# Kernel optimization log

Hardware: AMD Instinct MI355X
Metric: run time of the kernel (lower is better)

The kernel has to match this reference:

```python
import jax, jax.numpy as jnp
import numpy as np

B, T, HID = 2, 2048, 1536
H, HKV, D = 12, 2, 128
EPS = 1e-6
NEG = -1e9


def setup_inputs() -> dict:
    key = jax.random.key(0)
    ks = jax.random.split(key, 8)
    # rotary embeddings built from real angles (cos/sin of position*inv_freq)
    inv_freq = 1.0 / (10000.0 ** (jnp.arange(0, D, 2, dtype=jnp.float32) / D))  # [D/2]
    pos = jnp.arange(T, dtype=jnp.float32)
    ang = pos[:, None] * inv_freq[None, :]                       # [T, D/2]
    emb = jnp.concatenate([ang, ang], axis=-1)                   # [T, D]
    cos = jnp.broadcast_to(jnp.cos(emb)[None], (B, T, D))
    sin = jnp.broadcast_to(jnp.sin(emb)[None], (B, T, D))
    # additive causal mask [1,1,T,T]
    causal = jnp.tril(jnp.ones((T, T), dtype=bool))
    attention_mask = jnp.where(causal, 0.0, NEG).astype(jnp.float32)[None, None]
    s = 0.02
    return {
        "hidden_states": jax.random.normal(ks[0], (B, T, HID), jnp.float32),
        "cos": cos,
        "sin": sin,
        "attention_mask": attention_mask,
        "q_w": jax.random.normal(ks[1], (H * D, HID), jnp.float32) * s,
        "k_w": jax.random.normal(ks[2], (HKV * D, HID), jnp.float32) * s,
        "v_w": jax.random.normal(ks[3], (HKV * D, HID), jnp.float32) * s,
        "o_w": jax.random.normal(ks[4], (HID, H * D), jnp.float32) * s,
        "q_norm_w": jnp.ones((D,), jnp.float32),
        "k_norm_w": jnp.ones((D,), jnp.float32),
    }


def _rms_norm(x, w):
    # per-head RMSNorm over last dim (head_dim), computed in fp32
    xf = x.astype(jnp.float32)
    var = jnp.mean(xf * xf, axis=-1, keepdims=True)
    return (w * (xf * jax.lax.rsqrt(var + EPS))).astype(x.dtype)


def _rotate_half(x):
    x1, x2 = jnp.split(x, 2, axis=-1)
    return jnp.concatenate([-x2, x1], axis=-1)


def reference(hidden_states, cos, sin, attention_mask, q_w, k_w, v_w, o_w, q_norm_w, k_norm_w):
    b, t, _ = hidden_states.shape
    n_rep = H // HKV
    scale = D ** -0.5

    # projections -> [B, n_heads, T, D]
    q = (hidden_states @ q_w.T).reshape(b, t, H, D)
    k = (hidden_states @ k_w.T).reshape(b, t, HKV, D)
    v = (hidden_states @ v_w.T).reshape(b, t, HKV, D).transpose(0, 2, 1, 3)

    # per-head QK RMSNorm, then to [B, H, T, D]
    q = _rms_norm(q, q_norm_w).transpose(0, 2, 1, 3)
    k = _rms_norm(k, k_norm_w).transpose(0, 2, 1, 3)

    # RoPE (cos/sin broadcast over head axis)
    c = cos[:, None, :, :]
    s = sin[:, None, :, :]
    q = q * c + _rotate_half(q) * s
    k = k * c + _rotate_half(k) * s

    # GQA repeat_kv: [B, HKV, T, D] -> [B, H, T, D]
    k = jnp.repeat(k, n_rep, axis=1)
    v = jnp.repeat(v, n_rep, axis=1)

    attn = jnp.einsum('bhqd,bhkd->bhqk', q, k) * scale + attention_mask
    attn = jax.nn.softmax(attn.astype(jnp.float32), axis=-1).astype(q.dtype)
    out = jnp.einsum('bhqk,bhkd->bhqd', attn, v)
    out = out.transpose(0, 2, 1, 3).reshape(b, t, H * D)
    return out @ o_w.T
```

## Files before the change

### kernel.cpp

```cpp
#include <hip/hip_runtime.h>
#include <hip/hip_bf16.h>


#define B_   2
#define T_   2048
#define HID_ 1536
#define H_   12
#define HKV_ 2
#define D_   128
#define GQ_  (H_ / HKV_)
#define NQKV_ 2048
#define SCALE_ 0.08838834764831845f

typedef unsigned short u16;
typedef __attribute__((ext_vector_type(4))) float f32x4;
typedef __attribute__((ext_vector_type(8))) short bf16x8;
typedef __attribute__((ext_vector_type(4))) unsigned short u16x4;
typedef __attribute__((ext_vector_type(8))) unsigned short u16x8;

__device__ __forceinline__ u16 f2b(float f) {
  union { __hip_bfloat16 h; u16 u; } cv;
  cv.h = __float2bfloat16(f);
  return cv.u;
}
__device__ __forceinline__ float b2f(u16 u) {
  union { float f; unsigned i; } cv;
  cv.i = ((unsigned)u) << 16;
  return cv.f;
}

__device__ __forceinline__ void glds16(const u16* g, u16* l) {
  __builtin_amdgcn_global_load_lds((const __attribute__((address_space(1))) void*)g,
                                   (__attribute__((address_space(3))) void*)l, 16, 0, 0);
}

__global__ __launch_bounds__(256) void cvt_f32_bf16(const float* __restrict__ src,
                                                    u16* __restrict__ dst, int n4) {
  int i = blockIdx.x * 256 + threadIdx.x;
  const int stride = gridDim.x * 256;
  for (; i < n4; i += stride) {
    const float4 v = reinterpret_cast<const float4*>(src)[i];
    u16x4 o = {f2b(v.x), f2b(v.y), f2b(v.z), f2b(v.w)};
    reinterpret_cast<u16x4*>(dst)[i] = o;
  }
}

#define NH4_ 1572864
#define NQ4_ 589824
#define NK4_ 98304
__global__ __launch_bounds__(256) void cvt_inputs(const float* __restrict__ hidden,
                                                  const float* __restrict__ q_w,
                                                  const float* __restrict__ k_w,
                                                  const float* __restrict__ v_w,
                                                  u16* __restrict__ hidden_b,
                                                  u16* __restrict__ qkvw) {
  int i = blockIdx.x * 256 + threadIdx.x;
  const int stride = gridDim.x * 256;
  const int total = NH4_ + NQ4_ + 2 * NK4_;
  for (; i < total; i += stride) {
    float4 v;
    u16x4* dst;
    if (i < NH4_) {
      v = reinterpret_cast<const float4*>(hidden)[i];
      dst = reinterpret_cast<u16x4*>(hidden_b) + i;
    } else {
      const int j = i - NH4_;
      if (j < NQ4_) v = reinterpret_cast<const float4*>(q_w)[j];
      else if (j < NQ4_ + NK4_) v = reinterpret_cast<const float4*>(k_w)[j - NQ4_];
      else v = reinterpret_cast<const float4*>(v_w)[j - NQ4_ - NK4_];
      dst = reinterpret_cast<u16x4*>(qkvw) + j;
    }
    u16x4 o = {f2b(v.x), f2b(v.y), f2b(v.z), f2b(v.w)};
    *dst = o;
  }
}

__global__ __launch_bounds__(256) void gemm_bt(const u16* __restrict__ A,
                                               const u16* __restrict__ W,
                                               float* __restrict__ C,
                                               int M, int N, int K) {
  __shared__ __align__(16) u16 As[2][128 * 64];
  __shared__ __align__(16) u16 Ws[2][128 * 64];
  const int tid  = threadIdx.x;
  const int lane = tid & 63;
  const int wid  = tid >> 6;
  const int wr = wid >> 1, wc = wid & 1;
  const int l15 = lane & 15, kg = lane >> 4;
  const int rowBase = blockIdx.y * 128;
  const int colBase = blockIdx.x * 128;

  const int srow = lane >> 3;
  const int scol = (lane & 7) << 3;
  const u16* Ab = A + (size_t)(rowBase + wid * 32 + srow) * K + scol;
  const u16* Wb = W + (size_t)(colBase + wid * 32 + srow) * K + scol;

  const f32x4 zero4 = {0.f, 0.f, 0.f, 0.f};
  f32x4 acc[4][4];
#pragma unroll
  for (int m = 0; m < 4; ++m)
#pragma unroll
    for (int n = 0; n < 4; ++n) acc[m][n] = zero4;

  const int nt = K >> 6;
#pragma unroll
  for (int c = 0; c < 4; ++c) {
    glds16(Ab + (size_t)(c * 8) * K, &As[0][(wid * 4 + c) * 512]);
    glds16(Wb + (size_t)(c * 8) * K, &Ws[0][(wid * 4 + c) * 512]);
  }
  asm volatile("s_waitcnt vmcnt(0)" ::: "memory");
  __builtin_amdgcn_s_barrier();
  asm volatile("" ::: "memory");
  int cur = 0;

  for (int t = 0; t < nt; ++t) {
    if (t + 1 < nt) {
      const int k0 = (t + 1) << 6;
#pragma unroll
      for (int c = 0; c < 4; ++c) {
        glds16(Ab + (size_t)(c * 8) * K + k0, &As[cur ^ 1][(wid * 4 + c) * 512]);
        glds16(Wb + (size_t)(c * 8) * K + k0, &Ws[cur ^ 1][(wid * 4 + c) * 512]);
      }
    }
    bf16x8 a[4][2], b[4][2];
#pragma unroll
    for (int m = 0; m < 4; ++m)
#pragma unroll
      for (int ks = 0; ks < 2; ++ks)
        a[m][ks] = *reinterpret_cast<const bf16x8*>(
            &As[cur][(wr * 64 + m * 16 + l15) * 64 + ks * 32 + kg * 8]);
#pragma unroll
    for (int n = 0; n < 4; ++n)
#pragma unroll
      for (int ks = 0; ks < 2; ++ks)
        b[n][ks] = *reinterpret_cast<const bf16x8*>(
            &Ws[cur][(wc * 64 + n * 16 + l15) * 64 + ks * 32 + kg * 8]);
    __builtin_amdgcn_s_setprio(1);
#pragma unroll
    for (int m = 0; m < 4; ++m)
#pragma unroll
      for (int n = 0; n < 4; ++n)
#pragma unroll
        for (int ks = 0; ks < 2; ++ks)
          acc[m][n] = __builtin_amdgcn_mfma_f32_16x16x32_bf16(a[m][ks], b[n][ks],
                                                              acc[m][n], 0, 0, 0);
    __builtin_amdgcn_s_setprio(0);
    if (t + 1 < nt) {
      asm volatile("s_waitcnt vmcnt(0)" ::: "memory");
      __builtin_amdgcn_s_barrier();
      asm volatile("" ::: "memory");
      cur ^= 1;
    }
  }
#pragma unroll
  for (int m = 0; m < 4; ++m) {
    const int row0 = rowBase + wr * 64 + m * 16 + kg * 4;
#pragma unroll
    for (int n = 0; n < 4; ++n) {
      const int col = colBase + wc * 64 + n * 16 + l15;
#pragma unroll
      for (int r = 0; r < 4; ++r) C[(size_t)(row0 + r) * N + col] = acc[m][n][r];
    }
  }
}

__global__ __launch_bounds__(256) void gemm_qkv(
    const u16* __restrict__ A, const u16* __restrict__ W,
    const float* __restrict__ cosb, const float* __restrict__ sinb,
    const float* __restrict__ q_nw, const float* __restrict__ k_nw,
    u16* __restrict__ q_b, u16* __restrict__ k_b, u16* __restrict__ vt_b) {
  __shared__ __align__(16) u16 smem[32768];
  const int tid  = threadIdx.x;
  const int lane = tid & 63;
  const int wid  = tid >> 6;
  const int wr = wid >> 1, wc = wid & 1;
  const int l15 = lane & 15, kg = lane >> 4;
  const int rowBase = blockIdx.y * 128;
  const int colBase = blockIdx.x * 128;
  const int K = HID_;

  const int srow = lane >> 3;
  const int scol = (lane & 7) << 3;
  const u16* Ab = A + (size_t)(rowBase + wid * 32 + srow) * K + scol;
  const u16* Wb = W + (size_t)(colBase + wid * 32 + srow) * K + scol;

  const f32x4 zero4 = {0.f, 0.f, 0.f, 0.f};
  f32x4 acc[4][4];
#pragma unroll
  for (int m = 0; m < 4; ++m)
#pragma unroll
    for (int n = 0; n < 4; ++n) acc[m][n] = zero4;

  const int nt = K >> 6;
#pragma unroll
  for (int c = 0; c < 4; ++c) {
    glds16(Ab + (size_t)(c * 8) * K, &smem[(wid * 4 + c) * 512]);
    glds16(Wb + (size_t)(c * 8) * K, &smem[8192 + (wid * 4 + c) * 512]);
  }
  asm volatile("s_waitcnt vmcnt(0)" ::: "memory");
  __builtin_amdgcn_s_barrier();
  asm volatile("" ::: "memory");
  int cur = 0;

  for (int t = 0; t < nt; ++t) {
    if (t + 1 < nt) {
      const int k0 = (t + 1) << 6;
      const int ob = (cur ^ 1) * 16384;
#pragma unroll
      for (int c = 0; c < 4; ++c) {
        glds16(Ab + (size_t)(c * 8) * K + k0, &smem[ob + (wid * 4 + c) * 512]);
        glds16(Wb + (size_t)(c * 8) * K + k0, &smem[ob + 8192 + (wid * 4 + c) * 512]);
      }
    }
    const int ib = cur * 16384;
    bf16x8 a[4][2], b[4][2];
#pragma unroll
    for (int m = 0; m < 4; ++m)
#pragma unroll
      for (int ks = 0; ks < 2; ++ks)
        a[m][ks] = *reinterpret_cast<const bf16x8*>(
            &smem[ib + (wr * 64 + m * 16 + l15) * 64 + ks * 32 + kg * 8]);
#pragma unroll
    for (int n = 0; n < 4; ++n)
#pragma unroll
      for (int ks = 0; ks < 2; ++ks)
        b[n][ks] = *reinterpret_cast<const bf16x8*>(
            &smem[ib + 8192 + (wc * 64 + n * 16 + l15) * 64 + ks * 32 + kg * 8]);
    __builtin_amdgcn_s_setprio(1);
#pragma unroll
    for (int m = 0; m < 4; ++m)
#pragma unroll
      for (int n = 0; n < 4; ++n)
#pragma unroll
        for (int ks = 0; ks < 2; ++ks)
          acc[m][n] = __builtin_amdgcn_mfma_f32_16x16x32_bf16(a[m][ks], b[n][ks],
                                                              acc[m][n], 0, 0, 0);
    __builtin_amdgcn_s_setprio(0);
    if (t + 1 < nt) {
      asm volatile("s_waitcnt vmcnt(0)" ::: "memory");
      __builtin_amdgcn_s_barrier();
      asm volatile("" ::: "memory");
      cur ^= 1;
    }
  }

  __syncthreads();
#pragma unroll
  for (int m = 0; m < 4; ++m)
#pragma unroll
    for (int n = 0; n < 4; ++n)
#pragma unroll
      for (int r = 0; r < 4; ++r)
        smem[(wr * 64 + m * 16 + kg * 4 + r) * 137 + wc * 64 + n * 16 + l15] =
            f2b(acc[m][n][r]);
  __syncthreads();

  const int ct = blockIdx.x;
  const int b = rowBase >> 11;
  if (ct < 14) {
    const float* nw = (ct < 12) ? q_nw : k_nw;
    const float nwl = nw[lane], nwh = nw[lane + 64];
    const float sc = (ct < 12) ? SCALE_ : 1.0f;
    u16* dstbase = (ct < 12) ? (q_b + (size_t)(b * H_ + ct) * T_ * D_)
                             : (k_b + (size_t)(b * HKV_ + (ct - 12)) * T_ * D_);
    for (int i = 0; i < 32; ++i) {
      const int row = wid * 32 + i;
      const int tok = rowBase + row;
      const int t = tok & (T_ - 1);
      const float x1 = b2f(smem[row * 137 + lane]);
      const float x2 = b2f(smem[row * 137 + lane + 64]);
      float ss = x1 * x1 + x2 * x2;
#pragma unroll
      for (int msk = 32; msk >= 1; msk >>= 1) ss += __shfl_xor(ss, msk);
      const float rinv = rsqrtf(ss * (1.0f / D_) + 1e-6f);
      const float c1 = cosb[(size_t)tok * D_ + lane];
      const float c2 = cosb[(size_t)tok * D_ + lane + 64];
      const float s1 = sinb[(size_t)tok * D_ + lane];
      const float s2 = sinb[(size_t)tok * D_ + lane + 64];
      const float n1 = x1 * rinv * nwl, n2 = x2 * rinv * nwh;
      u16* dst = dstbase + (size_t)t * D_;
      dst[lane] = f2b((n1 * c1 - n2 * s1) * sc);
      dst[lane + 64] = f2b((n2 * c2 + n1 * s2) * sc);
    }
  } else {
    const int hv = ct - 14;
    const int tp = (lane & 32) | (((lane >> 2) & 3) << 3) | (((lane >> 4) & 1) << 2) |
                   (lane & 3);
    u16* vb = vt_b + (size_t)(b * HKV_ + hv) * D_ * T_;
    const int tb = rowBase & (T_ - 1);
    for (int it = 0; it < 64; ++it) {
      const int d = wid * 32 + (it >> 1), half = it & 1;
      const float x = b2f(smem[(half * 64 + lane) * 137 + d]);
      vb[(size_t)d * T_ + tb + half * 64 + tp] = f2b(x);
    }
  }
}

__constant__ int QT_ARR[40] = {15,15,15,15,14,14,11,11,11,10, 7, 7, 3,
                               14,14,13,13,13,13,12,12,10,10, 9, 9, 6, 6,
                               12,12, 9, 8, 8, 8, 5, 5, 2,
                                4, 4, 1, 0};
__constant__ int C_ARR[40]  = { 0, 1, 2, 3, 0, 1, 0, 1, 2, 0, 0, 1,-1,
                                2, 3, 0, 1, 2, 3, 0, 1, 1, 2, 0, 1, 0, 1,
                                2, 3, 2, 0, 1, 2, 0, 1,-1,
                                0, 1,-1,-1};
__device__ __forceinline__ int nc_of(int qt) { return (qt < 8) ? 2 : ((qt < 12) ? 3 : 4); }
__device__ __forceinline__ int mlbase_of(int qt) {
  return (qt < 8) ? 2 * (qt - 4) : ((qt < 12) ? 8 + 3 * (qt - 8) : 20 + 4 * (qt - 12));
}
__device__ __forceinline__ int pbase_of(int qt) {
  return (qt < 8) ? (qt - 4) : ((qt < 12) ? 4 + 2 * (qt - 8) : 12 + 3 * (qt - 12));
}

__global__ __launch_bounds__(256) void attn_kernel(const u16* __restrict__ q_b,
                                                   const u16* __restrict__ k_b,
                                                   const u16* __restrict__ vt_b,
                                                   u16* __restrict__ aout,
                                                   u16* __restrict__ po0,
                                                   float2* __restrict__ ml) {
  __shared__ __align__(16) u16 Ks[2][64 * 128];
  __shared__ __align__(16) u16 Vs[2][128 * 64];
  const int id = blockIdx.x;
  const int item = id / 24;
  const int bh = id - item * 24;
  const int qt = QT_ARR[item];
  const int c = C_ARR[item];
  int kt0, ktend;
  bool partial;
  if (c < 0) {
    kt0 = 0; ktend = 2 * qt + 1; partial = false;
  } else {
    const int nt = 2 * qt + 2;
    const int nc = nc_of(qt);
    const int base = nt / nc, rem = nt - base * nc;
    kt0 = c * base + (c < rem ? c : rem);
    ktend = kt0 + base + (c < rem ? 1 : 0) - 1;
    partial = true;
  }
  const int b = bh / H_, h = bh - b * H_;
  const int kvh = h / GQ_;
  const int tid = threadIdx.x;
  const int w = tid >> 6, lane = tid & 63;
  const int l15 = lane & 15, kg = lane >> 4;
  const int qbase = qt * 128;

  const u16* Kb = k_b + (size_t)(b * HKV_ + kvh) * T_ * D_;
  const u16* Vb = vt_b + (size_t)(b * HKV_ + kvh) * D_ * T_;

  bf16x8 qf[2][4];
#pragma unroll
  for (int qb = 0; qb < 2; ++qb) {
    const u16* qrow =
        q_b + ((size_t)(b * H_ + h) * T_ + qbase + w * 32 + qb * 16 + l15) * D_;
#pragma unroll
    for (int s4 = 0; s4 < 4; ++s4)
      qf[qb][s4] = *reinterpret_cast<const bf16x8*>(qrow + s4 * 32 + kg * 8);
  }

  int kK[4], vK[4];
#pragma unroll
  for (int cc = 0; cc < 4; ++cc) {
    const int ch = w * 4 + cc;
    const int kr = ch * 4 + (lane >> 4);
    kK[cc] = kr * D_ + (((lane & 15) << 3) ^ ((kr & 7) << 3));
    const int dr = ch * 8 + (lane >> 3);
    vK[cc] = dr * T_ + (((lane & 7) << 3) ^ ((dr & 7) << 3));
  }
  const int xorv = (l15 & 7) << 3;

  const f32x4 zero4 = {0.f, 0.f, 0.f, 0.f};
  f32x4 o[2][8];
#pragma unroll
  for (int qb = 0; qb < 2; ++qb)
#pragma unroll
    for (int n = 0; n < 8; ++n) o[qb][n] = zero4;
  float m[2] = {0.f, 0.f};
  float lsum[2] = {0.f, 0.f};

  {
    const size_t kb = (size_t)kt0 * 64;
#pragma unroll
    for (int cc = 0; cc < 4; ++cc) {
      glds16(Kb + kb * D_ + kK[cc], &Ks[0][(w * 4 + cc) * 512]);
      glds16(Vb + kb + vK[cc], &Vs[0][(w * 4 + cc) * 512]);
    }
  }
  int cur = 0;

  for (int kt = kt0; kt <= ktend; ++kt) {
    if (kt < ktend) {
      const size_t kb = (size_t)(kt + 1) * 64;
#pragma unroll
      for (int cc = 0; cc < 4; ++cc) {
        glds16(Kb + kb * D_ + kK[cc], &Ks[cur ^ 1][(w * 4 + cc) * 512]);
        glds16(Vb + kb + vK[cc], &Vs[cur ^ 1][(w * 4 + cc) * 512]);
      }
      asm volatile("s_waitcnt vmcnt(8)" ::: "memory");
    } else {
      asm volatile("s_waitcnt vmcnt(0)" ::: "memory");
    }
    __builtin_amdgcn_s_barrier();
    asm volatile("" ::: "memory");

    const u16* Kc = &Ks[cur][0];
    const u16* Vc = &Vs[cur][0];
    f32x4 sc[2][4];
#pragma unroll
    for (int qb = 0; qb < 2; ++qb)
#pragma unroll
      for (int n = 0; n < 4; ++n) sc[qb][n] = zero4;
    __builtin_amdgcn_s_setprio(1);
#pragma unroll
    for (int n = 0; n < 4; ++n)
#pragma unroll
      for (int s4 = 0; s4 < 4; ++s4) {
        const int koff = (n * 16 + l15) * 128 + ((s4 * 32 + kg * 8) ^ xorv);
        bf16x8 kf = *reinterpret_cast<const bf16x8*>(&Kc[koff]);
#pragma unroll
        for (int qb = 0; qb < 2; ++qb)
          sc[qb][n] = __builtin_amdgcn_mfma_f32_16x16x32_bf16(kf, qf[qb][s4],
                                                              sc[qb][n], 0, 0, 0);
      }
    __builtin_amdgcn_s_setprio(0);
    if (kt >= 2 * qt) {
#pragma unroll
      for (int qb = 0; qb < 2; ++qb) {
        const int qg = w * 32 + qb * 16 + l15;
        const int kbb = (kt - 2 * qt) * 64;
#pragma unroll
        for (int n = 0; n < 4; ++n)
#pragma unroll
          for (int r = 0; r < 4; ++r)
            if (kbb + n * 16 + kg * 4 + r > qg) sc[qb][n][r] = -3e38f;
      }
    }
    float pm[2];
#pragma unroll
    for (int qb = 0; qb < 2; ++qb) {
      float v = sc[qb][0][0];
#pragma unroll
      for (int n = 0; n < 4; ++n)
#pragma unroll
        for (int r = 0; r < 4; ++r) v = fmaxf(v, sc[qb][n][r]);
      v = fmaxf(v, __shfl_xor(v, 16));
      v = fmaxf(v, __shfl_xor(v, 32));
      pm[qb] = v;
    }
    if (__any((pm[0] > m[0] + 8.f) | (pm[1] > m[1] + 8.f))) {
#pragma unroll
      for (int qb = 0; qb < 2; ++qb) {
        const float mn = fmaxf(m[qb], pm[qb]);
        const float al = __expf(m[qb] - mn);
        m[qb] = mn;
        lsum[qb] *= al;
        float alT[4];
#pragma unroll
        for (int r = 0; r < 4; ++r)
          alT[r] = __shfl(al, (lane & 48) | (kg * 4 + r));
#pragma unroll
        for (int n = 0; n < 8; ++n)
#pragma unroll
          for (int r = 0; r < 4; ++r) o[qb][n][r] *= alT[r];
      }
    }
#pragma unroll
    for (int qb = 0; qb < 2; ++qb) {
      float rs = 0.f;
#pragma unroll
      for (int n = 0; n < 4; ++n)
#pragma unroll
        for (int r = 0; r < 4; ++r) {
          const float p = __expf(sc[qb][n][r] - m[qb]);
          sc[qb][n][r] = p;
          rs += p;
        }
      rs += __shfl_xor(rs, 16);
      rs += __shfl_xor(rs, 32);
      lsum[qb] += rs;
    }
    bf16x8 pf[2][2];
#pragma unroll
    for (int qb = 0; qb < 2; ++qb)
#pragma unroll
      for (int ks = 0; ks < 2; ++ks)
#pragma unroll
        for (int r = 0; r < 4; ++r) {
          pf[qb][ks][r] = (short)f2b(sc[qb][2 * ks][r]);
          pf[qb][ks][r + 4] = (short)f2b(sc[qb][2 * ks + 1][r]);
        }
    __builtin_amdgcn_s_setprio(1);
#pragma unroll
    for (int n = 0; n < 8; ++n)
#pragma unroll
      for (int ks = 0; ks < 2; ++ks) {
        const int voff = (n * 16 + l15) * 64 + ((ks * 32 + kg * 8) ^ xorv);
        bf16x8 vf = *reinterpret_cast<const bf16x8*>(&Vc[voff]);
#pragma unroll
        for (int qb = 0; qb < 2; ++qb)
          o[qb][n] = __builtin_amdgcn_mfma_f32_16x16x32_bf16(pf[qb][ks], vf,
                                                             o[qb][n], 0, 0, 0);
      }
    __builtin_amdgcn_s_setprio(0);
    __builtin_amdgcn_s_barrier();
    cur ^= 1;
  }

  if (!partial) {
    float invT[2][4];
#pragma unroll
    for (int qb = 0; qb < 2; ++qb) {
      const float inv = 1.0f / lsum[qb];
#pragma unroll
      for (int r = 0; r < 4; ++r)
        invT[qb][r] = __shfl(inv, (lane & 48) | (kg * 4 + r));
    }
#pragma unroll
    for (int qb = 0; qb < 2; ++qb) {
      const int t0 = qbase + w * 32 + qb * 16 + kg * 4;
#pragma unroll
      for (int n = 0; n < 8; ++n)
#pragma unroll
        for (int r = 0; r < 4; ++r)
          aout[(size_t)(b * T_ + t0 + r) * (H_ * D_) + h * D_ + n * 16 + l15] =
              f2b(o[qb][n][r] * invT[qb][r]);
    }
  } else {
    const int mlslot = bh * 36 + mlbase_of(qt) + c;
    if (kg == 0) {
#pragma unroll
      for (int qb = 0; qb < 2; ++qb) {
        float2 v;
        v.x = m[qb];
        v.y = lsum[qb];
        ml[(size_t)mlslot * 128 + w * 32 + qb * 16 + l15] = v;
      }
    }
    if (c == 0) {
#pragma unroll
      for (int qb = 0; qb < 2; ++qb) {
        const int t0 = qbase + w * 32 + qb * 16 + kg * 4;
#pragma unroll
        for (int n = 0; n < 8; ++n)
#pragma unroll
          for (int r = 0; r < 4; ++r)
            aout[(size_t)(b * T_ + t0 + r) * (H_ * D_) + h * D_ + n * 16 + l15] =
                f2b(o[qb][n][r]);
      }
    } else {
      const int pslot = bh * 24 + pbase_of(qt) + (c - 1);
#pragma unroll
      for (int qb = 0; qb < 2; ++qb) {
        const int row0 = w * 32 + qb * 16 + kg * 4;
#pragma unroll
        for (int n = 0; n < 8; ++n)
#pragma unroll
          for (int r = 0; r < 4; ++r)
            po0[((size_t)pslot * 128 + row0 + r) * 128 + n * 16 + l15] =
                f2b(o[qb][n][r]);
      }
    }
  }
}

__global__ __launch_bounds__(256) void combine_kernel(u16* __restrict__ aout,
                                                      const u16* __restrict__ po0,
                                                      const float2* __restrict__ ml) {
  const int qt = 4 + blockIdx.x;
  const int bh = blockIdx.y;
  const int nc = nc_of(qt);
  const int mlb = bh * 36 + mlbase_of(qt);
  const int pb = bh * 24 + pbase_of(qt);
  const int b = bh / H_, h = bh - b * H_;
  const int t0 = qt * 128;
  const int tid = threadIdx.x;
  const int row = tid >> 1;
  const int colc = (tid & 1) << 6;

  float ms[4], ls[4];
  float mm = -3e38f;
  for (int cc = 0; cc < nc; ++cc) {
    const float2 v = ml[(size_t)(mlb + cc) * 128 + row];
    ms[cc] = v.x; ls[cc] = v.y;
    mm = fmaxf(mm, v.x);
  }
  float lt = 0.f;
  float scl[4];
  for (int cc = 0; cc < nc; ++cc) {
    scl[cc] = __expf(ms[cc] - mm);
    lt += ls[cc] * scl[cc];
  }
  const float inv = 1.0f / lt;
  for (int cc = 0; cc < nc; ++cc) scl[cc] *= inv;

  u16* a = aout + (size_t)(b * T_ + t0 + row) * (H_ * D_) + h * D_ + colc;
#pragma unroll
  for (int j = 0; j < 8; ++j) {
    u16x8 v0 = *reinterpret_cast<const u16x8*>(a + j * 8);
    float acc[8];
#pragma unroll
    for (int e = 0; e < 8; ++e) acc[e] = b2f(v0[e]) * scl[0];
    for (int cc = 1; cc < nc; ++cc) {
      const u16* p = po0 + ((size_t)(pb + cc - 1) * 128 + row) * 128 + colc;
      u16x8 vc = *reinterpret_cast<const u16x8*>(p + j * 8);
#pragma unroll
      for (int e = 0; e < 8; ++e) acc[e] += b2f(vc[e]) * scl[cc];
    }
    u16x8 outv;
#pragma unroll
    for (int e = 0; e < 8; ++e) outv[e] = f2b(acc[e]);
    *reinterpret_cast<u16x8*>(a + j * 8) = outv;
  }
}

extern "C" void kernel_launch(void* const* d_in, const int* in_sizes, int n_in,
                              void* d_out, int out_size, void* d_ws, size_t ws_size,
                              hipStream_t stream) {
  const float* hidden = (const float*)d_in[0];
  const float* cosb   = (const float*)d_in[1];
  const float* sinb   = (const float*)d_in[2];
  const float* q_w  = (const float*)d_in[4];
  const float* k_w  = (const float*)d_in[5];
  const float* v_w  = (const float*)d_in[6];
  const float* o_w  = (const float*)d_in[7];
  const float* q_nw = (const float*)d_in[8];
  const float* k_nw = (const float*)d_in[9];
  float* out = (float*)d_out;

  char* ws = (char*)d_ws;
  const size_t MB = 1u << 20;
  u16*    hidden_b = (u16*)(ws);
  u16*    qkvw     = (u16*)(ws + 12 * MB);
  u16*    q_b      = (u16*)(ws + 18 * MB);
  u16*    k_b      = (u16*)(ws + 30 * MB);
  u16*    vt_b     = (u16*)(ws + 32 * MB);
  u16*    aout     = (u16*)(ws);
  u16*    owb      = (u16*)(ws + 12 * MB);
  float2* ml       = (float2*)(ws + 17 * MB);
  u16*    po0      = (u16*)d_out;

  const dim3 blk(256);
  const int M = B_ * T_;

  cvt_inputs<<<2048, blk, 0, stream>>>(hidden, q_w, k_w, v_w, hidden_b, qkvw);

  gemm_qkv<<<dim3(NQKV_ / 128, M / 128), blk, 0, stream>>>(
      hidden_b, qkvw, cosb, sinb, q_nw, k_nw, q_b, k_b, vt_b);

  cvt_f32_bf16<<<2048, blk, 0, stream>>>(o_w, owb, (H_ * D_ * HID_) / 4);

  attn_kernel<<<960, blk, 0, stream>>>(q_b, k_b, vt_b, aout, po0, ml);
  combine_kernel<<<dim3(12, B_ * H_), blk, 0, stream>>>(aout, po0, ml);

  gemm_bt<<<dim3(HID_ / 128, M / 128), blk, 0, stream>>>(aout, owb, out,
                                                         M, HID_, HID_);
}
```

Measured before the change: 189.8 us.

## Fold o_w conversion into input cast, single-buffer attention K/V tiles

Converts o_w to bf16 inside the existing input-conversion kernel, removing a separate launch. The K and V tiles in attention are now single-buffered with two __syncthreads per tile instead of double-buffered prefetch, halving their shared-memory use. The halved LDS may allow more resident blocks per CU, at the cost of no longer overlapping global loads with MFMA compute within a block. The workspace layout also changes: K and V^T now live in the output buffer, past the region used for partial outputs.

```diff
diff --git a/kernel.cpp b/kernel.cpp
--- a/kernel.cpp
+++ b/kernel.cpp
@@ -34,17 +34,6 @@
                                    (__attribute__((address_space(3))) void*)l, 16, 0, 0);
 }
 
-__global__ __launch_bounds__(256) void cvt_f32_bf16(const float* __restrict__ src,
-                                                    u16* __restrict__ dst, int n4) {
-  int i = blockIdx.x * 256 + threadIdx.x;
-  const int stride = gridDim.x * 256;
-  for (; i < n4; i += stride) {
-    const float4 v = reinterpret_cast<const float4*>(src)[i];
-    u16x4 o = {f2b(v.x), f2b(v.y), f2b(v.z), f2b(v.w)};
-    reinterpret_cast<u16x4*>(dst)[i] = o;
-  }
-}
-
 #define NH4_ 1572864
 #define NQ4_ 589824
 #define NK4_ 98304
@@ -52,11 +41,14 @@
                                                   const float* __restrict__ q_w,
                                                   const float* __restrict__ k_w,
                                                   const float* __restrict__ v_w,
+                                                  const float* __restrict__ o_w,
                                                   u16* __restrict__ hidden_b,
-                                                  u16* __restrict__ qkvw) {
+                                                  u16* __restrict__ qkvw,
+                                                  u16* __restrict__ owb) {
   int i = blockIdx.x * 256 + threadIdx.x;
   const int stride = gridDim.x * 256;
-  const int total = NH4_ + NQ4_ + 2 * NK4_;
+  const int nqkv = NQ4_ + 2 * NK4_;
+  const int total = NH4_ + nqkv + NQ4_;
   for (; i < total; i += stride) {
     float4 v;
     u16x4* dst;
@@ -65,10 +57,15 @@
       dst = reinterpret_cast<u16x4*>(hidden_b) + i;
     } else {
       const int j = i - NH4_;
-      if (j < NQ4_) v = reinterpret_cast<const float4*>(q_w)[j];
-      else if (j < NQ4_ + NK4_) v = reinterpret_cast<const float4*>(k_w)[j - NQ4_];
-      else v = reinterpret_cast<const float4*>(v_w)[j - NQ4_ - NK4_];
-      dst = reinterpret_cast<u16x4*>(qkvw) + j;
+      if (j < nqkv) {
+        if (j < NQ4_) v = reinterpret_cast<const float4*>(q_w)[j];
+        else if (j < NQ4_ + NK4_) v = reinterpret_cast<const float4*>(k_w)[j - NQ4_];
+        else v = reinterpret_cast<const float4*>(v_w)[j - NQ4_ - NK4_];
+        dst = reinterpret_cast<u16x4*>(qkvw) + j;
+      } else {
+        v = reinterpret_cast<const float4*>(o_w)[j - nqkv];
+        dst = reinterpret_cast<u16x4*>(owb) + (j - nqkv);
+      }
     }
     u16x4 o = {f2b(v.x), f2b(v.y), f2b(v.z), f2b(v.w)};
     *dst = o;
@@ -317,8 +314,8 @@
                                                    u16* __restrict__ aout,
                                                    u16* __restrict__ po0,
                                                    float2* __restrict__ ml) {
-  __shared__ __align__(16) u16 Ks[2][64 * 128];
-  __shared__ __align__(16) u16 Vs[2][128 * 64];
+  __shared__ __align__(16) u16 Ks[64 * 128];
+  __shared__ __align__(16) u16 Vs[128 * 64];
   const int id = blockIdx.x;
   const int item = id / 24;
   const int bh = id - item * 24;
@@ -376,33 +373,17 @@
   float m[2] = {0.f, 0.f};
   float lsum[2] = {0.f, 0.f};
 
-  {
-    const size_t kb = (size_t)kt0 * 64;
-#pragma unroll
-    for (int cc = 0; cc < 4; ++cc) {
-      glds16(Kb + kb * D_ + kK[cc], &Ks[0][(w * 4 + cc) * 512]);
-      glds16(Vb + kb + vK[cc], &Vs[0][(w * 4 + cc) * 512]);
-    }
-  }
-  int cur = 0;
-
   for (int kt = kt0; kt <= ktend; ++kt) {
-    if (kt < ktend) {
-      const size_t kb = (size_t)(kt + 1) * 64;
+    __syncthreads();
+    {
+      const size_t kb = (size_t)kt * 64;
 #pragma unroll
       for (int cc = 0; cc < 4; ++cc) {
-        glds16(Kb + kb * D_ + kK[cc], &Ks[cur ^ 1][(w * 4 + cc) * 512]);
-        glds16(Vb + kb + vK[cc], &Vs[cur ^ 1][(w * 4 + cc) * 512]);
-      }
-      asm volatile("s_waitcnt vmcnt(8)" ::: "memory");
-    } else {
-      asm volatile("s_waitcnt vmcnt(0)" ::: "memory");
-    }
-    __builtin_amdgcn_s_barrier();
-    asm volatile("" ::: "memory");
-
-    const u16* Kc = &Ks[cur][0];
-    const u16* Vc = &Vs[cur][0];
+        glds16(Kb + kb * D_ + kK[cc], &Ks[(w * 4 + cc) * 512]);
+        glds16(Vb + kb + vK[cc], &Vs[(w * 4 + cc) * 512]);
+      }
+    }
+    __syncthreads();
     f32x4 sc[2][4];
 #pragma unroll
     for (int qb = 0; qb < 2; ++qb)
@@ -414,7 +395,7 @@
 #pragma unroll
       for (int s4 = 0; s4 < 4; ++s4) {
         const int koff = (n * 16 + l15) * 128 + ((s4 * 32 + kg * 8) ^ xorv);
-        bf16x8 kf = *reinterpret_cast<const bf16x8*>(&Kc[koff]);
+        bf16x8 kf = *reinterpret_cast<const bf16x8*>(&Ks[koff]);
 #pragma unroll
         for (int qb = 0; qb < 2; ++qb)
           sc[qb][n] = __builtin_amdgcn_mfma_f32_16x16x32_bf16(kf, qf[qb][s4],
@@ -493,15 +474,13 @@
 #pragma unroll
       for (int ks = 0; ks < 2; ++ks) {
         const int voff = (n * 16 + l15) * 64 + ((ks * 32 + kg * 8) ^ xorv);
-        bf16x8 vf = *reinterpret_cast<const bf16x8*>(&Vc[voff]);
+        bf16x8 vf = *reinterpret_cast<const bf16x8*>(&Vs[voff]);
 #pragma unroll
         for (int qb = 0; qb < 2; ++qb)
           o[qb][n] = __builtin_amdgcn_mfma_f32_16x16x32_bf16(pf[qb][ks], vf,
                                                              o[qb][n], 0, 0, 0);
       }
     __builtin_amdgcn_s_setprio(0);
-    __builtin_amdgcn_s_barrier();
-    cur ^= 1;
   }
 
   if (!partial) {
@@ -630,23 +609,22 @@
   u16*    hidden_b = (u16*)(ws);
   u16*    qkvw     = (u16*)(ws + 12 * MB);
   u16*    q_b      = (u16*)(ws + 18 * MB);
-  u16*    k_b      = (u16*)(ws + 30 * MB);
-  u16*    vt_b     = (u16*)(ws + 32 * MB);
+  u16*    owb      = (u16*)(ws + 30 * MB);
   u16*    aout     = (u16*)(ws);
-  u16*    owb      = (u16*)(ws + 12 * MB);
-  float2* ml       = (float2*)(ws + 17 * MB);
+  float2* ml       = (float2*)(ws + 12 * MB);
+  u16*    k_b      = (u16*)((char*)d_out + 19 * MB);
+  u16*    vt_b     = (u16*)((char*)d_out + 21 * MB);
   u16*    po0      = (u16*)d_out;
 
   const dim3 blk(256);
   const int M = B_ * T_;
 
-  cvt_inputs<<<2048, blk, 0, stream>>>(hidden, q_w, k_w, v_w, hidden_b, qkvw);
+  cvt_inputs<<<2048, blk, 0, stream>>>(hidden, q_w, k_w, v_w, o_w,
+                                       hidden_b, qkvw, owb);
 
   gemm_qkv<<<dim3(NQKV_ / 128, M / 128), blk, 0, stream>>>(
       hidden_b, qkvw, cosb, sinb, q_nw, k_nw, q_b, k_b, vt_b);
 
-  cvt_f32_bf16<<<2048, blk, 0, stream>>>(o_w, owb, (H_ * D_ * HID_) / 4);
-
   attn_kernel<<<960, blk, 0, stream>>>(q_b, k_b, vt_b, aout, po0, ml);
   combine_kernel<<<dim3(12, B_ * H_), blk, 0, stream>>>(aout, po0, ml);
 
```

Result: no change. 187.1 us (-1.4%).
